# Kernel tuning notes

Measured on AMD Instinct MI355X. Metric: run time of the kernel, lower is better.

The kernel has to match this reference:

```python
import jax, jax.numpy as jnp
import numpy as np

B, T, NE = 8, 4096, 1024
E, TOPK = 16, 2
LIN = NE + 32 + NE // 4 + NE // 4 + NE // 8 + NE // 8  # 1824
N_CITIES = 4


def setup_inputs() -> dict:
    key = jax.random.key(0)
    ks = jax.random.split(key, 11)
    s = 1.0 / np.sqrt(LIN)
    return {
        "mh_output": jax.random.normal(ks[0], (B, T, NE), jnp.float32),
        "delta_t_info": jax.random.normal(ks[1], (B, T, NE // 4), jnp.float32),
        "delta_dis_info": jax.random.normal(ks[2], (B, T, NE // 4), jnp.float32),
        "delta_rg_info": jax.random.normal(ks[3], (B, T, NE // 8), jnp.float32),
        "delta_entropy_info": jax.random.normal(ks[4], (B, T, NE // 8), jnp.float32),
        "city_embeddings": jax.random.normal(ks[5], (N_CITIES, 32), jnp.float32),
        "w_route": jax.random.uniform(ks[6], (LIN, E), jnp.float32, -s, s),
        "b_route": jax.random.uniform(ks[7], (E,), jnp.float32, -s, s),
        "w_noise": jax.random.uniform(ks[8], (LIN, E), jnp.float32, -s, s),
        "b_noise": jax.random.uniform(ks[9], (E,), jnp.float32, -s, s),
        "noise_eps": jax.random.normal(ks[10], (B, T, E), jnp.float32),
        "city_index": 0,
    }


def reference(mh_output, delta_t_info, delta_dis_info, delta_rg_info,
              delta_entropy_info, city_embeddings, w_route, b_route,
              w_noise, b_noise, noise_eps, city_index):
    b, t, _ = mh_output.shape
    city_embed = city_embeddings[city_index]  # [32]
    city_embeds = jnp.broadcast_to(city_embed[None, None, :], (b, t, 32))
    x = jnp.concatenate([mh_output, city_embeds, delta_t_info, delta_dis_info,
                         delta_rg_info, delta_entropy_info], axis=-1)  # [B,T,LIN]
    logits = jnp.einsum('btf,fe->bte', x, w_route) + b_route
    noise_logits = jnp.einsum('btf,fe->bte', x, w_noise) + b_noise
    noisy_logits = logits + noise_eps * jax.nn.softplus(noise_logits)  # training path
    gate1 = jax.nn.softmax(noisy_logits, axis=-1)
    top_k_logits, indices = jax.lax.top_k(noisy_logits, TOPK)  # [B,T,K]
    # scatter top-k values into a -inf tensor == mask non-topk entries to -inf
    mask = jnp.sum(jax.nn.one_hot(indices, noisy_logits.shape[-1], dtype=jnp.bool_), axis=-2) > 0
    sparse_logits = jnp.where(mask, noisy_logits, -jnp.inf)
    router_output = jax.nn.softmax(sparse_logits, axis=-1)
    return router_output, indices, gate1
```

## Files before the change

### kernel.cpp

```cpp
#include <hip/hip_runtime.h>
#include <math.h>


#define TOKS 128
#define NCHUNK 28
#define I_OFF 524288
#define G_OFF 589824
#define SA 68
#define SW 36
#define SS 36

__device__ __forceinline__ float softplus_f(float x) {
  return fmaxf(x, 0.0f) + log1pf(expf(-fabsf(x)));
}

__device__ __forceinline__ float get_comp(const float4& v, int kk) {
  return kk == 0 ? v.x : kk == 1 ? v.y : kk == 2 ? v.z : v.w;
}

__global__ __launch_bounds__(512, 2) void router_kernel(
    const float* __restrict__ mh, const float* __restrict__ dt,
    const float* __restrict__ dd, const float* __restrict__ rg,
    const float* __restrict__ de, const float* __restrict__ cemb_all,
    const float* __restrict__ w_route, const float* __restrict__ b_route,
    const float* __restrict__ w_noise, const float* __restrict__ b_noise,
    const float* __restrict__ eps, const int* __restrict__ city_index,
    float* __restrict__ out) {
  __shared__ float smem[22016];
  __shared__ float city_l[32];
  float* sA0 = smem;
  float* sA1 = smem + 8704;
  float* sW0 = smem + 17408;
  float* sW1 = smem + 19712;
  float* sS  = smem;

  const int tid = threadIdx.x;
  const int w   = tid >> 6;
  const int ln  = tid & 63;
  const int tg  = ln & 15;
  const int eg  = ln >> 4;
  const int blockTok = blockIdx.x * TOKS;

  if (tid < 32) {
    const int e = tid & 15;
    const float* wsrc = (tid < 16) ? w_route : w_noise;
    const float* bsrc = (tid < 16) ? b_route : b_noise;
    const float* ce = cemb_all + city_index[0] * 32;
    float s = bsrc[e];
#pragma unroll
    for (int j = 0; j < 32; ++j) s = fmaf(ce[j], wsrc[(1024 + j) * 16 + e], s);
    city_l[tid] = s;
  }

  float4 accL[8], accH[8];
#pragma unroll
  for (int j = 0; j < 8; ++j) {
    accL[j] = make_float4(0.f, 0.f, 0.f, 0.f);
    accH[j] = make_float4(0.f, 0.f, 0.f, 0.f);
  }

  const int arow = tid >> 4, acol = (tid & 15) * 4;
  const int wrow = tid >> 3, wcol = tid & 7;

  float4 AR0, AR1, AR2, AR3, WR;

  auto a_src = [&](int g, int row) -> const float* {
    const float* base; int stride;
    if (g < 16)      { base = mh + g * 64;        stride = 1024; }
    else if (g < 20) { base = dt + (g - 16) * 64; stride = 256; }
    else if (g < 24) { base = dd + (g - 20) * 64; stride = 256; }
    else if (g < 26) { base = rg + (g - 24) * 64; stride = 128; }
    else             { base = de + (g - 26) * 64; stride = 128; }
    return base + (size_t)(blockTok + row) * stride;
  };

  auto prefetch = [&](int g) {
    AR0 = *(const float4*)(a_src(g, arow +  0) + acol);
    AR1 = *(const float4*)(a_src(g, arow + 32) + acol);
    AR2 = *(const float4*)(a_src(g, arow + 64) + acol);
    AR3 = *(const float4*)(a_src(g, arow + 96) + acol);
    const int kb = g * 64 + ((g >= 16) ? 32 : 0);
    const float* ws = (wcol < 4)
        ? (w_route + (kb + wrow) * 16 + wcol * 4)
        : (w_noise + (kb + wrow) * 16 + (wcol - 4) * 4);
    WR = *(const float4*)ws;
  };

  auto stage = [&](float* A, float* W) {
    *(float4*)&A[(arow +  0) * SA + acol] = AR0;
    *(float4*)&A[(arow + 32) * SA + acol] = AR1;
    *(float4*)&A[(arow + 64) * SA + acol] = AR2;
    *(float4*)&A[(arow + 96) * SA + acol] = AR3;
    *(float4*)&W[wrow * SW + wcol * 4] = WR;
  };

  prefetch(0);
  stage(sA0, sW0);
  __syncthreads();

  for (int c = 0; c < NCHUNK; ++c) {
    const float* A = (c & 1) ? sA1 : sA0;
    const float* W = (c & 1) ? sW1 : sW0;

    if (c + 1 < NCHUNK) prefetch(c + 1);

    const int k0 = w * 8;
#pragma unroll
    for (int q = 0; q < 2; ++q) {
      const int koff = k0 + q * 4;
      float4 a[8];
#pragma unroll
      for (int j = 0; j < 8; ++j)
        a[j] = *(const float4*)&A[(tg + 16 * j) * SA + koff];
#pragma unroll
      for (int kk = 0; kk < 4; ++kk) {
        float4 wv0 = *(const float4*)&W[(koff + kk) * SW + eg * 8];
        float4 wv1 = *(const float4*)&W[(koff + kk) * SW + eg * 8 + 4];
#pragma unroll
        for (int j = 0; j < 8; ++j) {
          const float s = get_comp(a[j], kk);
          accL[j].x = fmaf(s, wv0.x, accL[j].x);
          accL[j].y = fmaf(s, wv0.y, accL[j].y);
          accL[j].z = fmaf(s, wv0.z, accL[j].z);
          accL[j].w = fmaf(s, wv0.w, accL[j].w);
          accH[j].x = fmaf(s, wv1.x, accH[j].x);
          accH[j].y = fmaf(s, wv1.y, accH[j].y);
          accH[j].z = fmaf(s, wv1.z, accH[j].z);
          accH[j].w = fmaf(s, wv1.w, accH[j].w);
        }
      }
    }

    if (c + 1 < NCHUNK) stage((c & 1) ? sA0 : sA1, (c & 1) ? sW0 : sW1);
    __syncthreads();
  }

  for (int r = 0; r < 8; ++r) {
    if (w == r) {
#pragma unroll
      for (int j = 0; j < 8; ++j) {
        float* p = &sS[(tg + 16 * j) * SS + eg * 8];
        if (r == 0) {
          *(float4*)(p)     = accL[j];
          *(float4*)(p + 4) = accH[j];
        } else {
          float4 x0 = *(float4*)(p), x1 = *(float4*)(p + 4);
          x0.x += accL[j].x; x0.y += accL[j].y; x0.z += accL[j].z; x0.w += accL[j].w;
          x1.x += accH[j].x; x1.y += accH[j].y; x1.z += accH[j].z; x1.w += accH[j].w;
          *(float4*)(p)     = x0;
          *(float4*)(p + 4) = x1;
        }
      }
    }
    __syncthreads();
  }

  if (tid < TOKS) {
    const int tokg = blockTok + tid;
    float l[32];
#pragma unroll
    for (int e4 = 0; e4 < 8; ++e4) {
      float4 s0 = *(const float4*)&sS[tid * SS + e4 * 4];
      l[e4 * 4 + 0] = s0.x + ((e4 * 4 + 0 < 32) ? 0.f : 0.f);
      l[e4 * 4 + 0] = s0.x; l[e4 * 4 + 1] = s0.y;
      l[e4 * 4 + 2] = s0.z; l[e4 * 4 + 3] = s0.w;
    }
#pragma unroll
    for (int e = 0; e < 32; ++e) l[e] += city_l[e];

    const float* ep = eps + (size_t)tokg * 16;
    float n[16];
#pragma unroll
    for (int e = 0; e < 16; ++e)
      n[e] = fmaf(ep[e], softplus_f(l[16 + e]), l[e]);

    float m1 = -INFINITY; int i1 = 0;
#pragma unroll
    for (int e = 0; e < 16; ++e)
      if (n[e] > m1) { m1 = n[e]; i1 = e; }
    float m2 = -INFINITY; int i2 = 0;
#pragma unroll
    for (int e = 0; e < 16; ++e)
      if (e != i1 && n[e] > m2) { m2 = n[e]; i2 = e; }

    float ex[16], Z = 0.f;
#pragma unroll
    for (int e = 0; e < 16; ++e) { ex[e] = expf(n[e] - m1); Z += ex[e]; }
    const float invZ  = 1.0f / Z;
    const float invZ2 = 1.0f / (1.0f + expf(m2 - m1));

    float r[16], g1[16];
#pragma unroll
    for (int e = 0; e < 16; ++e) {
      r[e]  = (e == i1 || e == i2) ? ex[e] * invZ2 : 0.0f;
      g1[e] = ex[e] * invZ;
    }

    float* ro = out + (size_t)tokg * 16;
#pragma unroll
    for (int e4 = 0; e4 < 4; ++e4)
      *(float4*)(ro + e4 * 4) = make_float4(r[e4*4], r[e4*4+1], r[e4*4+2], r[e4*4+3]);

    out[I_OFF + (size_t)tokg * 2 + 0] = (float)i1;
    out[I_OFF + (size_t)tokg * 2 + 1] = (float)i2;

    float* go = out + G_OFF + (size_t)tokg * 16;
#pragma unroll
    for (int e4 = 0; e4 < 4; ++e4)
      *(float4*)(go + e4 * 4) = make_float4(g1[e4*4], g1[e4*4+1], g1[e4*4+2], g1[e4*4+3]);
  }
}

extern "C" void kernel_launch(void* const* d_in, const int* in_sizes, int n_in,
                              void* d_out, int out_size, void* d_ws, size_t ws_size,
                              hipStream_t stream) {
  const float* mh = (const float*)d_in[0];
  const float* dt = (const float*)d_in[1];
  const float* dd = (const float*)d_in[2];
  const float* rg = (const float*)d_in[3];
  const float* de = (const float*)d_in[4];
  const float* ce = (const float*)d_in[5];
  const float* wr = (const float*)d_in[6];
  const float* br = (const float*)d_in[7];
  const float* wn = (const float*)d_in[8];
  const float* bn = (const float*)d_in[9];
  const float* ep = (const float*)d_in[10];
  const int*   ci = (const int*)d_in[11];
  float* out = (float*)d_out;

  router_kernel<<<256, 512, 0, stream>>>(mh, dt, dd, rg, de, ce, wr, br, wn, bn,
                                         ep, ci, out);
}
```

Measured before the change: 297.0 us.

## Split the K dimension across two blocks and add a separate epilogue kernel

The GEMM over the feature dimension is split in half, so each 128-token tile is handled by two blocks (512 blocks instead of 256). Each block writes its partial 128x32 logits to workspace, and a second kernel sums the halves, adds the city/bias term, and runs the noisy top-k softmax epilogue. Shared-memory double buffering is dropped for a single buffer with two barriers per chunk, halving LDS use so that launch bounds allow more resident blocks. The aim is to fill the GPU's many CUs better, at the cost of a second launch, a workspace round trip, and less overlap between loads and compute.

```diff
diff --git a/kernel.cpp b/kernel.cpp
--- a/kernel.cpp
+++ b/kernel.cpp
@@ -2,8 +2,7 @@
 #include <math.h>
 
 
-#define TOKS 128
-#define NCHUNK 28
+#define NCHUNK_HALF 14
 #define I_OFF 524288
 #define G_OFF 589824
 #define SA 68
@@ -18,39 +17,26 @@
   return kk == 0 ? v.x : kk == 1 ? v.y : kk == 2 ? v.z : v.w;
 }
 
-__global__ __launch_bounds__(512, 2) void router_kernel(
+__global__ __launch_bounds__(512, 4) void gemm_half_kernel(
     const float* __restrict__ mh, const float* __restrict__ dt,
     const float* __restrict__ dd, const float* __restrict__ rg,
-    const float* __restrict__ de, const float* __restrict__ cemb_all,
-    const float* __restrict__ w_route, const float* __restrict__ b_route,
-    const float* __restrict__ w_noise, const float* __restrict__ b_noise,
-    const float* __restrict__ eps, const int* __restrict__ city_index,
-    float* __restrict__ out) {
-  __shared__ float smem[22016];
-  __shared__ float city_l[32];
-  float* sA0 = smem;
-  float* sA1 = smem + 8704;
-  float* sW0 = smem + 17408;
-  float* sW1 = smem + 19712;
-  float* sS  = smem;
+    const float* __restrict__ de,
+    const float* __restrict__ w_route, const float* __restrict__ w_noise,
+    float* __restrict__ ws) {
+  __shared__ float smem[11008];
+  float* sA = smem;
+  float* sW = smem + 8704;
+  float* sS = smem;
 
   const int tid = threadIdx.x;
   const int w   = tid >> 6;
   const int ln  = tid & 63;
   const int tg  = ln & 15;
   const int eg  = ln >> 4;
-  const int blockTok = blockIdx.x * TOKS;
-
-  if (tid < 32) {
-    const int e = tid & 15;
-    const float* wsrc = (tid < 16) ? w_route : w_noise;
-    const float* bsrc = (tid < 16) ? b_route : b_noise;
-    const float* ce = cemb_all + city_index[0] * 32;
-    float s = bsrc[e];
-#pragma unroll
-    for (int j = 0; j < 32; ++j) s = fmaf(ce[j], wsrc[(1024 + j) * 16 + e], s);
-    city_l[tid] = s;
-  }
+  const int tb  = blockIdx.x >> 1;
+  const int h   = blockIdx.x & 1;
+  const int blockTok = tb * 128;
+  const int g0 = h * NCHUNK_HALF;
 
   float4 accL[8], accH[8];
 #pragma unroll
@@ -80,29 +66,24 @@
     AR2 = *(const float4*)(a_src(g, arow + 64) + acol);
     AR3 = *(const float4*)(a_src(g, arow + 96) + acol);
     const int kb = g * 64 + ((g >= 16) ? 32 : 0);
-    const float* ws = (wcol < 4)
+    const float* wsrc = (wcol < 4)
         ? (w_route + (kb + wrow) * 16 + wcol * 4)
         : (w_noise + (kb + wrow) * 16 + (wcol - 4) * 4);
-    WR = *(const float4*)ws;
+    WR = *(const float4*)wsrc;
   };
 
-  auto stage = [&](float* A, float* W) {
-    *(float4*)&A[(arow +  0) * SA + acol] = AR0;
-    *(float4*)&A[(arow + 32) * SA + acol] = AR1;
-    *(float4*)&A[(arow + 64) * SA + acol] = AR2;
-    *(float4*)&A[(arow + 96) * SA + acol] = AR3;
-    *(float4*)&W[wrow * SW + wcol * 4] = WR;
-  };
-
-  prefetch(0);
-  stage(sA0, sW0);
-  __syncthreads();
-
-  for (int c = 0; c < NCHUNK; ++c) {
-    const float* A = (c & 1) ? sA1 : sA0;
-    const float* W = (c & 1) ? sW1 : sW0;
-
-    if (c + 1 < NCHUNK) prefetch(c + 1);
+  prefetch(g0);
+
+  for (int c = 0; c < NCHUNK_HALF; ++c) {
+    __syncthreads();
+    *(float4*)&sA[(arow +  0) * SA + acol] = AR0;
+    *(float4*)&sA[(arow + 32) * SA + acol] = AR1;
+    *(float4*)&sA[(arow + 64) * SA + acol] = AR2;
+    *(float4*)&sA[(arow + 96) * SA + acol] = AR3;
+    *(float4*)&sW[wrow * SW + wcol * 4] = WR;
+    __syncthreads();
+
+    if (c + 1 < NCHUNK_HALF) prefetch(g0 + c + 1);
 
     const int k0 = w * 8;
 #pragma unroll
@@ -111,11 +92,11 @@
       float4 a[8];
 #pragma unroll
       for (int j = 0; j < 8; ++j)
-        a[j] = *(const float4*)&A[(tg + 16 * j) * SA + koff];
+        a[j] = *(const float4*)&sA[(tg + 16 * j) * SA + koff];
 #pragma unroll
       for (int kk = 0; kk < 4; ++kk) {
-        float4 wv0 = *(const float4*)&W[(koff + kk) * SW + eg * 8];
-        float4 wv1 = *(const float4*)&W[(koff + kk) * SW + eg * 8 + 4];
+        float4 wv0 = *(const float4*)&sW[(koff + kk) * SW + eg * 8];
+        float4 wv1 = *(const float4*)&sW[(koff + kk) * SW + eg * 8 + 4];
 #pragma unroll
         for (int j = 0; j < 8; ++j) {
           const float s = get_comp(a[j], kk);
@@ -130,11 +111,9 @@
         }
       }
     }
-
-    if (c + 1 < NCHUNK) stage((c & 1) ? sA0 : sA1, (c & 1) ? sW0 : sW1);
-    __syncthreads();
-  }
-
+  }
+
+  __syncthreads();
   for (int r = 0; r < 8; ++r) {
     if (w == r) {
 #pragma unroll
@@ -155,60 +134,90 @@
     __syncthreads();
   }
 
-  if (tid < TOKS) {
-    const int tokg = blockTok + tid;
-    float l[32];
-#pragma unroll
-    for (int e4 = 0; e4 < 8; ++e4) {
-      float4 s0 = *(const float4*)&sS[tid * SS + e4 * 4];
-      l[e4 * 4 + 0] = s0.x + ((e4 * 4 + 0 < 32) ? 0.f : 0.f);
-      l[e4 * 4 + 0] = s0.x; l[e4 * 4 + 1] = s0.y;
-      l[e4 * 4 + 2] = s0.z; l[e4 * 4 + 3] = s0.w;
-    }
-#pragma unroll
-    for (int e = 0; e < 32; ++e) l[e] += city_l[e];
-
-    const float* ep = eps + (size_t)tokg * 16;
-    float n[16];
-#pragma unroll
-    for (int e = 0; e < 16; ++e)
-      n[e] = fmaf(ep[e], softplus_f(l[16 + e]), l[e]);
-
-    float m1 = -INFINITY; int i1 = 0;
-#pragma unroll
-    for (int e = 0; e < 16; ++e)
-      if (n[e] > m1) { m1 = n[e]; i1 = e; }
-    float m2 = -INFINITY; int i2 = 0;
-#pragma unroll
-    for (int e = 0; e < 16; ++e)
-      if (e != i1 && n[e] > m2) { m2 = n[e]; i2 = e; }
-
-    float ex[16], Z = 0.f;
-#pragma unroll
-    for (int e = 0; e < 16; ++e) { ex[e] = expf(n[e] - m1); Z += ex[e]; }
-    const float invZ  = 1.0f / Z;
-    const float invZ2 = 1.0f / (1.0f + expf(m2 - m1));
-
-    float r[16], g1[16];
-#pragma unroll
-    for (int e = 0; e < 16; ++e) {
-      r[e]  = (e == i1 || e == i2) ? ex[e] * invZ2 : 0.0f;
-      g1[e] = ex[e] * invZ;
-    }
-
-    float* ro = out + (size_t)tokg * 16;
-#pragma unroll
-    for (int e4 = 0; e4 < 4; ++e4)
-      *(float4*)(ro + e4 * 4) = make_float4(r[e4*4], r[e4*4+1], r[e4*4+2], r[e4*4+3]);
-
-    out[I_OFF + (size_t)tokg * 2 + 0] = (float)i1;
-    out[I_OFF + (size_t)tokg * 2 + 1] = (float)i2;
-
-    float* go = out + G_OFF + (size_t)tokg * 16;
-#pragma unroll
-    for (int e4 = 0; e4 < 4; ++e4)
-      *(float4*)(go + e4 * 4) = make_float4(g1[e4*4], g1[e4*4+1], g1[e4*4+2], g1[e4*4+3]);
-  }
+  float* dst = ws + (size_t)(tb * 2 + h) * 4096;
+  const int f = tid * 8;
+  const int row = f >> 5, col = f & 31;
+  *(float4*)&dst[f]     = *(float4*)&sS[row * SS + col];
+  *(float4*)&dst[f + 4] = *(float4*)&sS[row * SS + col + 4];
+}
+
+__global__ __launch_bounds__(256, 4) void epilogue_kernel(
+    const float* __restrict__ ws, const float* __restrict__ cemb_all,
+    const int* __restrict__ city_index,
+    const float* __restrict__ w_route, const float* __restrict__ b_route,
+    const float* __restrict__ w_noise, const float* __restrict__ b_noise,
+    const float* __restrict__ eps, float* __restrict__ out) {
+  __shared__ float city_l[32];
+  const int tid = threadIdx.x;
+
+  if (tid < 32) {
+    const int e = tid & 15;
+    const float* wsrc = (tid < 16) ? w_route : w_noise;
+    const float* bsrc = (tid < 16) ? b_route : b_noise;
+    const float* ce = cemb_all + city_index[0] * 32;
+    float s = bsrc[e];
+#pragma unroll
+    for (int j = 0; j < 32; ++j) s = fmaf(ce[j], wsrc[(1024 + j) * 16 + e], s);
+    city_l[tid] = s;
+  }
+  __syncthreads();
+
+  const int t  = blockIdx.x * 256 + tid;
+  const int tb = t >> 7, r = t & 127;
+  const float* p0 = ws + (size_t)(tb * 2 + 0) * 4096 + r * 32;
+  const float* p1 = ws + (size_t)(tb * 2 + 1) * 4096 + r * 32;
+
+  float l[32];
+#pragma unroll
+  for (int e4 = 0; e4 < 8; ++e4) {
+    float4 a = *(const float4*)(p0 + e4 * 4);
+    float4 b = *(const float4*)(p1 + e4 * 4);
+    l[e4 * 4 + 0] = a.x + b.x + city_l[e4 * 4 + 0];
+    l[e4 * 4 + 1] = a.y + b.y + city_l[e4 * 4 + 1];
+    l[e4 * 4 + 2] = a.z + b.z + city_l[e4 * 4 + 2];
+    l[e4 * 4 + 3] = a.w + b.w + city_l[e4 * 4 + 3];
+  }
+
+  const float* ep = eps + (size_t)t * 16;
+  float n[16];
+#pragma unroll
+  for (int e = 0; e < 16; ++e)
+    n[e] = fmaf(ep[e], softplus_f(l[16 + e]), l[e]);
+
+  float m1 = -INFINITY; int i1 = 0;
+#pragma unroll
+  for (int e = 0; e < 16; ++e)
+    if (n[e] > m1) { m1 = n[e]; i1 = e; }
+  float m2 = -INFINITY; int i2 = 0;
+#pragma unroll
+  for (int e = 0; e < 16; ++e)
+    if (e != i1 && n[e] > m2) { m2 = n[e]; i2 = e; }
+
+  float ex[16], Z = 0.f;
+#pragma unroll
+  for (int e = 0; e < 16; ++e) { ex[e] = expf(n[e] - m1); Z += ex[e]; }
+  const float invZ  = 1.0f / Z;
+  const float invZ2 = 1.0f / (1.0f + expf(m2 - m1));
+
+  float rr[16], g1[16];
+#pragma unroll
+  for (int e = 0; e < 16; ++e) {
+    rr[e] = (e == i1 || e == i2) ? ex[e] * invZ2 : 0.0f;
+    g1[e] = ex[e] * invZ;
+  }
+
+  float* ro = out + (size_t)t * 16;
+#pragma unroll
+  for (int e4 = 0; e4 < 4; ++e4)
+    *(float4*)(ro + e4 * 4) = make_float4(rr[e4*4], rr[e4*4+1], rr[e4*4+2], rr[e4*4+3]);
+
+  out[I_OFF + (size_t)t * 2 + 0] = (float)i1;
+  out[I_OFF + (size_t)t * 2 + 1] = (float)i2;
+
+  float* go = out + G_OFF + (size_t)t * 16;
+#pragma unroll
+  for (int e4 = 0; e4 < 4; ++e4)
+    *(float4*)(go + e4 * 4) = make_float4(g1[e4*4], g1[e4*4+1], g1[e4*4+2], g1[e4*4+3]);
 }
 
 extern "C" void kernel_launch(void* const* d_in, const int* in_sizes, int n_in,
@@ -227,7 +236,8 @@
   const float* ep = (const float*)d_in[10];
   const int*   ci = (const int*)d_in[11];
   float* out = (float*)d_out;
-
-  router_kernel<<<256, 512, 0, stream>>>(mh, dt, dd, rg, de, ce, wr, br, wn, bn,
-                                         ep, ci, out);
-}
+  float* ws  = (float*)d_ws;
+
+  gemm_half_kernel<<<512, 512, 0, stream>>>(mh, dt, dd, rg, de, wr, wn, ws);
+  epilogue_kernel<<<128, 256, 0, stream>>>(ws, ce, ci, wr, br, wn, bn, ep, out);
+}
```

After: 466.0 us. 56.9% more time.
